# Kernel optimization log

Hardware: AMD Instinct MI355X
Metric: run time of the kernel (lower is better)

The kernel has to match this reference:

```python
import jax, jax.numpy as jnp
import numpy as np

B, H, S, D = 16, 12, 1024, 64  # batch, heads, seq, head_dim (dim=768, num_head=12)


def setup_inputs() -> dict:
    key = jax.random.key(0)
    ks = jax.random.split(key, 9)
    sc = 1.0 / np.sqrt(D)
    return {
        "x": jax.random.normal(ks[0], (B, H, S, D), dtype=jnp.float32),
        "Wq": jax.random.normal(ks[1], (D, D), dtype=jnp.float32) * sc,
        "bq": jax.random.normal(ks[2], (D,), dtype=jnp.float32) * 0.02,
        "Wk": jax.random.normal(ks[3], (D, D), dtype=jnp.float32) * sc,
        "bk": jax.random.normal(ks[4], (D,), dtype=jnp.float32) * 0.02,
        "Wv": jax.random.normal(ks[5], (D, D), dtype=jnp.float32) * sc,
        "bv": jax.random.normal(ks[6], (D,), dtype=jnp.float32) * 0.02,
        "Wo": jax.random.normal(ks[7], (D, D), dtype=jnp.float32) * sc,
        "bo": jax.random.normal(ks[8], (D,), dtype=jnp.float32) * 0.02,
    }


def reference(x, Wq, bq, Wk, bk, Wv, bv, Wo, bo):
    # torch Linear: y = x @ W^T + b, applied to last dim (head_dim)
    q = jnp.einsum("bhsd,ed->bhse", x, Wq) + bq
    k = jnp.einsum("bhsd,ed->bhse", x, Wk) + bk
    v = jnp.einsum("bhsd,ed->bhse", x, Wv) + bv
    scores = jnp.einsum("bhqd,bhkd->bhqk", q, k) / jnp.sqrt(jnp.float32(q.shape[-1]))
    attn = jax.nn.softmax(scores, axis=-1)
    out = jnp.einsum("bhqk,bhkd->bhqd", attn, v)
    out = jnp.einsum("bhsd,ed->bhse", out, Wo) + bo
    return out
```

## Files before the change

### kernel.cpp

```cpp
#include <hip/hip_runtime.h>
#include <math.h>


typedef __bf16 bf16x8 __attribute__((ext_vector_type(8)));
typedef float  f32x4  __attribute__((ext_vector_type(4)));

#define MFMA(a, b, c) __builtin_amdgcn_mfma_f32_16x16x32_bf16((a), (b), (c), 0, 0, 0)

static constexpr int S = 1024;
static constexpr int PAD = 72;
static constexpr size_t NE = 196608ull * 64ull;
static constexpr float QSCALE = 0.125f * 1.4426950408889634f;

__device__ inline unsigned long long pack4bf(float a, float b, float c, float d) {
    union { __bf16 h[4]; unsigned long long u; } pk;
    pk.h[0] = (__bf16)a; pk.h[1] = (__bf16)b; pk.h[2] = (__bf16)c; pk.h[3] = (__bf16)d;
    return pk.u;
}

union frag_u { bf16x8 v; unsigned long long u[2]; };

__global__ __launch_bounds__(256, 3) void proj(
    const float* __restrict__ x,
    const float* __restrict__ Wq, const float* __restrict__ bq,
    const float* __restrict__ Wk, const float* __restrict__ bk,
    const float* __restrict__ Wv, const float* __restrict__ bv,
    __bf16* __restrict__ gq, __bf16* __restrict__ gk, __bf16* __restrict__ gvt)
{
    __shared__ __align__(16) __bf16 lx[128][PAD];
    __shared__ __align__(16) __bf16 lbuf[128][PAD];
    __shared__ __align__(16) __bf16 lw[3][8][64][8];
    __shared__ float lb[3][64];

    const int tid = threadIdx.x;
    const int row_base = blockIdx.x * 128;

    #pragma unroll
    for (int i = tid * 4; i < 8192; i += 1024) {
        float4 v = *(const float4*)(x + (size_t)row_base * 64 + i);
        int r = i >> 6, c = i & 63;
        *(unsigned long long*)&lx[r][c] = pack4bf(v.x, v.y, v.z, v.w);
    }
    #pragma unroll
    for (int c = tid; c < 1536; c += 256) {
        int mtx = c >> 9, rest = c & 511;
        int fe = rest >> 6, ln = rest & 63;
        int mm = ln & 15, qq = ln >> 4;
        int et = fe >> 1, half = fe & 1;
        const float* src = (mtx == 0 ? Wq : mtx == 1 ? Wk : Wv)
                           + (size_t)(et * 16 + mm) * 64 + half * 32 + qq * 8;
        float4 u0 = *(const float4*)(src);
        float4 u1 = *(const float4*)(src + 4);
        *(unsigned long long*)&lw[mtx][fe][ln][0] = pack4bf(u0.x, u0.y, u0.z, u0.w);
        *(unsigned long long*)&lw[mtx][fe][ln][4] = pack4bf(u1.x, u1.y, u1.z, u1.w);
    }
    if (tid < 64) { lb[0][tid] = bq[tid]; lb[1][tid] = bk[tid]; lb[2][tid] = bv[tid]; }
    __syncthreads();

    const int w = tid >> 6, lane = tid & 63, m = lane & 15, quad = lane >> 4;
    const int bh = row_base >> 10;
    const int s_base = row_base & 1023;

    bf16x8 xf[2][2];
    #pragma unroll
    for (int g = 0; g < 2; g++) {
        xf[g][0] = *(const bf16x8*)&lx[w * 32 + g * 16 + m][quad * 8];
        xf[g][1] = *(const bf16x8*)&lx[w * 32 + g * 16 + m][32 + quad * 8];
    }

    #pragma unroll
    for (int mtx = 0; mtx < 2; mtx++) {
        #pragma unroll
        for (int et = 0; et < 4; et++) {
            bf16x8 wf0 = *(const bf16x8*)&lw[mtx][et * 2 + 0][lane][0];
            bf16x8 wf1 = *(const bf16x8*)&lw[mtx][et * 2 + 1][lane][0];
            float4 bias = *(const float4*)&lb[mtx][et * 16 + quad * 4];
            #pragma unroll
            for (int g = 0; g < 2; g++) {
                f32x4 acc = {0.f, 0.f, 0.f, 0.f};
                acc = MFMA(wf0, xf[g][0], acc);
                acc = MFMA(wf1, xf[g][1], acc);
                unsigned long long u;
                if (mtx == 0)
                    u = pack4bf((acc[0] + bias.x) * QSCALE, (acc[1] + bias.y) * QSCALE,
                                (acc[2] + bias.z) * QSCALE, (acc[3] + bias.w) * QSCALE);
                else
                    u = pack4bf(acc[0] + bias.x, acc[1] + bias.y,
                                acc[2] + bias.z, acc[3] + bias.w);
                *(unsigned long long*)&lbuf[w * 32 + g * 16 + m][et * 16 + quad * 4] = u;
            }
        }
        __syncthreads();
        __bf16* dst = (mtx == 0 ? gq : gk);
        #pragma unroll
        for (int it = 0; it < 4; it++) {
            int idx = it * 256 + tid;
            int row = idx >> 3, col = (idx & 7) * 8;
            *(uint4*)(dst + ((size_t)row_base + row) * 64 + col) = *(uint4*)&lbuf[row][col];
        }
        __syncthreads();
    }

    __bf16 (*lvt)[136] = (__bf16(*)[136])&lbuf[0][0];
    #pragma unroll
    for (int et = 0; et < 4; et++) {
        bf16x8 wf0 = *(const bf16x8*)&lw[2][et * 2 + 0][lane][0];
        bf16x8 wf1 = *(const bf16x8*)&lw[2][et * 2 + 1][lane][0];
        const float bias = lb[2][et * 16 + m];
        #pragma unroll
        for (int g = 0; g < 2; g++) {
            f32x4 acc = {0.f, 0.f, 0.f, 0.f};
            acc = MFMA(xf[g][0], wf0, acc);
            acc = MFMA(xf[g][1], wf1, acc);
            const int tp = (2 * w + g) & 3;
            const int p0 = 64 * (w >> 1) + 32 * (tp >> 1) + 8 * quad + 4 * (tp & 1);
            *(unsigned long long*)&lvt[et * 16 + m][p0] =
                pack4bf(acc[0] + bias, acc[1] + bias, acc[2] + bias, acc[3] + bias);
        }
    }
    __syncthreads();
    #pragma unroll
    for (int it = 0; it < 4; it++) {
        int idx = it * 256 + tid;
        int row = idx >> 4, col = (idx & 15) * 8;
        *(uint4*)(gvt + ((size_t)bh * 64 + row) * 1024 + s_base + col) = *(uint4*)&lvt[row][col];
    }
}

__global__ __launch_bounds__(256, 3) void attn(
    const __bf16* __restrict__ gq, const __bf16* __restrict__ gk,
    const __bf16* __restrict__ gvt, const float* __restrict__ Wo,
    const float* __restrict__ bo, float* __restrict__ out)
{
    __shared__ __align__(16) __bf16 lk[64][PAD];
    __shared__ __align__(16) __bf16 lv[64][PAD];

    const int tid = threadIdx.x;
    const int w = tid >> 6, lane = tid & 63, m = lane & 15, quad = lane >> 4;
    const int bh = blockIdx.x;
    const int q0 = blockIdx.y * 256 + w * 64;

    bf16x8 qf[4][2];
    #pragma unroll
    for (int g = 0; g < 4; g++) {
        const __bf16* qrow = gq + ((size_t)bh * S + q0 + g * 16 + m) * 64;
        qf[g][0] = *(const bf16x8*)(qrow + quad * 8);
        qf[g][1] = *(const bf16x8*)(qrow + 32 + quad * 8);
    }

    f32x4 o[4][4];
    float lsum[4] = {0.f, 0.f, 0.f, 0.f};
    #pragma unroll
    for (int g = 0; g < 4; g++)
        #pragma unroll
        for (int n = 0; n < 4; n++) o[g][n] = {0.f, 0.f, 0.f, 0.f};

    const int sr = tid >> 3;
    const int sc = (tid & 7) * 8;
    const __bf16* kbase = gk + (size_t)bh * S * 64;
    const __bf16* vbase = gvt + (size_t)bh * 64 * 1024;

    for (int kb = 0; kb < 16; kb++) {
        __syncthreads();
        {
            const int nb = kb * 64;
            uint4 k0 = *(const uint4*)(kbase + (size_t)(nb + sr) * 64 + sc);
            uint4 k1 = *(const uint4*)(kbase + (size_t)(nb + sr + 32) * 64 + sc);
            uint4 v0 = *(const uint4*)(vbase + (size_t)sr * 1024 + nb + sc);
            uint4 v1 = *(const uint4*)(vbase + (size_t)(sr + 32) * 1024 + nb + sc);
            *(uint4*)&lk[sr][sc]      = k0;
            *(uint4*)&lk[sr + 32][sc] = k1;
            *(uint4*)&lv[sr][sc]      = v0;
            *(uint4*)&lv[sr + 32][sc] = v1;
        }
        __syncthreads();

        __builtin_amdgcn_s_setprio(1);
        #pragma unroll
        for (int gp = 0; gp < 2; gp++) {
            frag_u pb[2][2];
            #pragma unroll
            for (int t = 0; t < 4; t++) {
                bf16x8 ka0 = *(const bf16x8*)&lk[t * 16 + m][quad * 8];
                bf16x8 ka1 = *(const bf16x8*)&lk[t * 16 + m][32 + quad * 8];
                #pragma unroll
                for (int gl = 0; gl < 2; gl++) {
                    const int g = gp * 2 + gl;
                    f32x4 acc = {0.f, 0.f, 0.f, 0.f};
                    acc = MFMA(ka0, qf[g][0], acc);
                    acc = MFMA(ka1, qf[g][1], acc);
                    float e0 = __builtin_amdgcn_exp2f(acc[0]);
                    float e1 = __builtin_amdgcn_exp2f(acc[1]);
                    float e2 = __builtin_amdgcn_exp2f(acc[2]);
                    float e3 = __builtin_amdgcn_exp2f(acc[3]);
                    lsum[g] += (e0 + e1) + (e2 + e3);
                    pb[gl][t >> 1].u[t & 1] = pack4bf(e0, e1, e2, e3);
                }
            }
            #pragma unroll
            for (int n = 0; n < 4; n++) {
                bf16x8 va0 = *(const bf16x8*)&lv[n * 16 + m][quad * 8];
                bf16x8 va1 = *(const bf16x8*)&lv[n * 16 + m][32 + quad * 8];
                #pragma unroll
                for (int gl = 0; gl < 2; gl++) {
                    const int g = gp * 2 + gl;
                    o[g][n] = MFMA(va0, pb[gl][0].v, o[g][n]);
                    o[g][n] = MFMA(va1, pb[gl][1].v, o[g][n]);
                }
            }
        }
        __builtin_amdgcn_s_setprio(0);
    }

    #pragma unroll
    for (int g = 0; g < 4; g++) {
        lsum[g] += __shfl_xor(lsum[g], 16);
        lsum[g] += __shfl_xor(lsum[g], 32);
    }

    bf16x8 wf[4][2];
    #pragma unroll
    for (int et = 0; et < 4; et++) {
        const float* worow = Wo + (size_t)(et * 16 + m) * 64;
        float4 c0 = *(const float4*)(worow + 4 * quad);
        float4 c1 = *(const float4*)(worow + 16 + 4 * quad);
        float4 c2 = *(const float4*)(worow + 32 + 4 * quad);
        float4 c3 = *(const float4*)(worow + 48 + 4 * quad);
        frag_u f0, f1;
        f0.u[0] = pack4bf(c0.x, c0.y, c0.z, c0.w);
        f0.u[1] = pack4bf(c1.x, c1.y, c1.z, c1.w);
        f1.u[0] = pack4bf(c2.x, c2.y, c2.z, c2.w);
        f1.u[1] = pack4bf(c3.x, c3.y, c3.z, c3.w);
        wf[et][0] = f0.v;
        wf[et][1] = f1.v;
    }
    float biasr[4];
    #pragma unroll
    for (int et = 0; et < 4; et++) biasr[et] = bo[et * 16 + m];

    #pragma unroll
    for (int g = 0; g < 4; g++) {
        const float inv = 1.f / lsum[g];
        frag_u af0, af1;
        af0.u[0] = pack4bf(o[g][0][0] * inv, o[g][0][1] * inv, o[g][0][2] * inv, o[g][0][3] * inv);
        af0.u[1] = pack4bf(o[g][1][0] * inv, o[g][1][1] * inv, o[g][1][2] * inv, o[g][1][3] * inv);
        af1.u[0] = pack4bf(o[g][2][0] * inv, o[g][2][1] * inv, o[g][2][2] * inv, o[g][2][3] * inv);
        af1.u[1] = pack4bf(o[g][3][0] * inv, o[g][3][1] * inv, o[g][3][2] * inv, o[g][3][3] * inv);
        #pragma unroll
        for (int et = 0; et < 4; et++) {
            f32x4 acc = {0.f, 0.f, 0.f, 0.f};
            acc = MFMA(af0.v, wf[et][0], acc);
            acc = MFMA(af1.v, wf[et][1], acc);
            #pragma unroll
            for (int r = 0; r < 4; r++) {
                size_t row = (size_t)bh * S + q0 + g * 16 + quad * 4 + r;
                out[row * 64 + et * 16 + m] = acc[r] + biasr[et];
            }
        }
    }
}

extern "C" void kernel_launch(void* const* d_in, const int* in_sizes, int n_in,
                              void* d_out, int out_size, void* d_ws, size_t ws_size,
                              hipStream_t stream) {
    const float* x  = (const float*)d_in[0];
    const float* Wq = (const float*)d_in[1];
    const float* bq = (const float*)d_in[2];
    const float* Wk = (const float*)d_in[3];
    const float* bk = (const float*)d_in[4];
    const float* Wv = (const float*)d_in[5];
    const float* bv = (const float*)d_in[6];
    const float* Wo = (const float*)d_in[7];
    const float* bo = (const float*)d_in[8];
    float* out = (float*)d_out;

    __bf16* gq  = (__bf16*)d_ws;
    __bf16* gk  = gq + NE;
    __bf16* gvt = gk + NE;

    proj<<<1536, 256, 0, stream>>>(x, Wq, bq, Wk, bk, Wv, bv, gq, gk, gvt);
    attn<<<dim3(192, 4), 256, 0, stream>>>(gq, gk, gvt, Wo, bo, out);
}
```

Measured before the change: 231.5 us.

## Fuse Q projection into attention kernel and double threads per block

The Q projection moves out of the projection kernel and into the attention kernel. Each attention block now loads its x rows, projects them to Q in shared memory with MFMA, and keeps Q in registers, so Q is never written to or read back from global memory. The attention block grows to 512 threads, with each wave handling 32 query rows instead of 64, which halves per-wave accumulator registers and lets one K/V tile load feed twice as many waves. The trade-off is that every attention block now loads and converts Wq and x itself, and each wave has less work per K/V tile to hide latency with.

Result: faster. 207.3 us (-10.5%).

```diff
diff --git a/kernel.cpp b/kernel.cpp
--- a/kernel.cpp
+++ b/kernel.cpp
@@ -20,17 +20,16 @@
 
 union frag_u { bf16x8 v; unsigned long long u[2]; };
 
-__global__ __launch_bounds__(256, 3) void proj(
+__global__ __launch_bounds__(256, 3) void projkv(
     const float* __restrict__ x,
-    const float* __restrict__ Wq, const float* __restrict__ bq,
     const float* __restrict__ Wk, const float* __restrict__ bk,
     const float* __restrict__ Wv, const float* __restrict__ bv,
-    __bf16* __restrict__ gq, __bf16* __restrict__ gk, __bf16* __restrict__ gvt)
+    __bf16* __restrict__ gk, __bf16* __restrict__ gvt)
 {
     __shared__ __align__(16) __bf16 lx[128][PAD];
     __shared__ __align__(16) __bf16 lbuf[128][PAD];
-    __shared__ __align__(16) __bf16 lw[3][8][64][8];
-    __shared__ float lb[3][64];
+    __shared__ __align__(16) __bf16 lw[2][8][64][8];
+    __shared__ float lb[2][64];
 
     const int tid = threadIdx.x;
     const int row_base = blockIdx.x * 128;
@@ -42,19 +41,18 @@
         *(unsigned long long*)&lx[r][c] = pack4bf(v.x, v.y, v.z, v.w);
     }
     #pragma unroll
-    for (int c = tid; c < 1536; c += 256) {
+    for (int c = tid; c < 1024; c += 256) {
         int mtx = c >> 9, rest = c & 511;
         int fe = rest >> 6, ln = rest & 63;
         int mm = ln & 15, qq = ln >> 4;
         int et = fe >> 1, half = fe & 1;
-        const float* src = (mtx == 0 ? Wq : mtx == 1 ? Wk : Wv)
-                           + (size_t)(et * 16 + mm) * 64 + half * 32 + qq * 8;
+        const float* src = (mtx ? Wv : Wk) + (size_t)(et * 16 + mm) * 64 + half * 32 + qq * 8;
         float4 u0 = *(const float4*)(src);
         float4 u1 = *(const float4*)(src + 4);
         *(unsigned long long*)&lw[mtx][fe][ln][0] = pack4bf(u0.x, u0.y, u0.z, u0.w);
         *(unsigned long long*)&lw[mtx][fe][ln][4] = pack4bf(u1.x, u1.y, u1.z, u1.w);
     }
-    if (tid < 64) { lb[0][tid] = bq[tid]; lb[1][tid] = bk[tid]; lb[2][tid] = bv[tid]; }
+    if (tid < 64) { lb[0][tid] = bk[tid]; lb[1][tid] = bv[tid]; }
     __syncthreads();
 
     const int w = tid >> 6, lane = tid & 63, m = lane & 15, quad = lane >> 4;
@@ -69,44 +67,35 @@
     }
 
     #pragma unroll
-    for (int mtx = 0; mtx < 2; mtx++) {
-        #pragma unroll
-        for (int et = 0; et < 4; et++) {
-            bf16x8 wf0 = *(const bf16x8*)&lw[mtx][et * 2 + 0][lane][0];
-            bf16x8 wf1 = *(const bf16x8*)&lw[mtx][et * 2 + 1][lane][0];
-            float4 bias = *(const float4*)&lb[mtx][et * 16 + quad * 4];
-            #pragma unroll
-            for (int g = 0; g < 2; g++) {
-                f32x4 acc = {0.f, 0.f, 0.f, 0.f};
-                acc = MFMA(wf0, xf[g][0], acc);
-                acc = MFMA(wf1, xf[g][1], acc);
-                unsigned long long u;
-                if (mtx == 0)
-                    u = pack4bf((acc[0] + bias.x) * QSCALE, (acc[1] + bias.y) * QSCALE,
-                                (acc[2] + bias.z) * QSCALE, (acc[3] + bias.w) * QSCALE);
-                else
-                    u = pack4bf(acc[0] + bias.x, acc[1] + bias.y,
-                                acc[2] + bias.z, acc[3] + bias.w);
-                *(unsigned long long*)&lbuf[w * 32 + g * 16 + m][et * 16 + quad * 4] = u;
-            }
-        }
-        __syncthreads();
-        __bf16* dst = (mtx == 0 ? gq : gk);
-        #pragma unroll
-        for (int it = 0; it < 4; it++) {
-            int idx = it * 256 + tid;
-            int row = idx >> 3, col = (idx & 7) * 8;
-            *(uint4*)(dst + ((size_t)row_base + row) * 64 + col) = *(uint4*)&lbuf[row][col];
-        }
-        __syncthreads();
-    }
+    for (int et = 0; et < 4; et++) {
+        bf16x8 wf0 = *(const bf16x8*)&lw[0][et * 2 + 0][lane][0];
+        bf16x8 wf1 = *(const bf16x8*)&lw[0][et * 2 + 1][lane][0];
+        float4 bias = *(const float4*)&lb[0][et * 16 + quad * 4];
+        #pragma unroll
+        for (int g = 0; g < 2; g++) {
+            f32x4 acc = {0.f, 0.f, 0.f, 0.f};
+            acc = MFMA(wf0, xf[g][0], acc);
+            acc = MFMA(wf1, xf[g][1], acc);
+            *(unsigned long long*)&lbuf[w * 32 + g * 16 + m][et * 16 + quad * 4] =
+                pack4bf(acc[0] + bias.x, acc[1] + bias.y,
+                        acc[2] + bias.z, acc[3] + bias.w);
+        }
+    }
+    __syncthreads();
+    #pragma unroll
+    for (int it = 0; it < 4; it++) {
+        int idx = it * 256 + tid;
+        int row = idx >> 3, col = (idx & 7) * 8;
+        *(uint4*)(gk + ((size_t)row_base + row) * 64 + col) = *(uint4*)&lbuf[row][col];
+    }
+    __syncthreads();
 
     __bf16 (*lvt)[136] = (__bf16(*)[136])&lbuf[0][0];
     #pragma unroll
     for (int et = 0; et < 4; et++) {
-        bf16x8 wf0 = *(const bf16x8*)&lw[2][et * 2 + 0][lane][0];
-        bf16x8 wf1 = *(const bf16x8*)&lw[2][et * 2 + 1][lane][0];
-        const float bias = lb[2][et * 16 + m];
+        bf16x8 wf0 = *(const bf16x8*)&lw[1][et * 2 + 0][lane][0];
+        bf16x8 wf1 = *(const bf16x8*)&lw[1][et * 2 + 1][lane][0];
+        const float bias = lb[1][et * 16 + m];
         #pragma unroll
         for (int g = 0; g < 2; g++) {
             f32x4 acc = {0.f, 0.f, 0.f, 0.f};
@@ -127,31 +116,76 @@
     }
 }
 
-__global__ __launch_bounds__(256, 3) void attn(
-    const __bf16* __restrict__ gq, const __bf16* __restrict__ gk,
-    const __bf16* __restrict__ gvt, const float* __restrict__ Wo,
-    const float* __restrict__ bo, float* __restrict__ out)
+__global__ __launch_bounds__(512, 4) void attn(
+    const float* __restrict__ x,
+    const float* __restrict__ Wq, const float* __restrict__ bq,
+    const __bf16* __restrict__ gk, const __bf16* __restrict__ gvt,
+    const float* __restrict__ Wo, const float* __restrict__ bo,
+    float* __restrict__ out)
 {
-    __shared__ __align__(16) __bf16 lk[64][PAD];
-    __shared__ __align__(16) __bf16 lv[64][PAD];
+    __shared__ __align__(16) union {
+        __bf16 xq[256][PAD];
+        struct {
+            __bf16 k[64][PAD];
+            __bf16 v[64][PAD];
+        } m;
+    } L;
 
     const int tid = threadIdx.x;
     const int w = tid >> 6, lane = tid & 63, m = lane & 15, quad = lane >> 4;
     const int bh = blockIdx.x;
-    const int q0 = blockIdx.y * 256 + w * 64;
-
-    bf16x8 qf[4][2];
-    #pragma unroll
-    for (int g = 0; g < 4; g++) {
-        const __bf16* qrow = gq + ((size_t)bh * S + q0 + g * 16 + m) * 64;
-        qf[g][0] = *(const bf16x8*)(qrow + quad * 8);
-        qf[g][1] = *(const bf16x8*)(qrow + 32 + quad * 8);
-    }
-
-    f32x4 o[4][4];
-    float lsum[4] = {0.f, 0.f, 0.f, 0.f};
-    #pragma unroll
-    for (int g = 0; g < 4; g++)
+    const int q0 = blockIdx.y * 256 + w * 32;
+
+    const float* xq32 = x + ((size_t)bh * 1024 + blockIdx.y * 256) * 64;
+    #pragma unroll
+    for (int i = tid * 4; i < 16384; i += 2048) {
+        float4 v = *(const float4*)(xq32 + i);
+        int r = i >> 6, c = i & 63;
+        *(unsigned long long*)&L.xq[r][c] = pack4bf(v.x, v.y, v.z, v.w);
+    }
+    __syncthreads();
+
+    bf16x8 xqf[2][2];
+    #pragma unroll
+    for (int g = 0; g < 2; g++) {
+        xqf[g][0] = *(const bf16x8*)&L.xq[w * 32 + g * 16 + m][quad * 8];
+        xqf[g][1] = *(const bf16x8*)&L.xq[w * 32 + g * 16 + m][32 + quad * 8];
+    }
+    #pragma unroll
+    for (int et = 0; et < 4; et++) {
+        const float* wqrow = Wq + (size_t)(et * 16 + m) * 64;
+        float4 a0 = *(const float4*)(wqrow + quad * 8);
+        float4 a1 = *(const float4*)(wqrow + quad * 8 + 4);
+        float4 a2 = *(const float4*)(wqrow + 32 + quad * 8);
+        float4 a3 = *(const float4*)(wqrow + 36 + quad * 8);
+        frag_u wf0, wf1;
+        wf0.u[0] = pack4bf(a0.x, a0.y, a0.z, a0.w);
+        wf0.u[1] = pack4bf(a1.x, a1.y, a1.z, a1.w);
+        wf1.u[0] = pack4bf(a2.x, a2.y, a2.z, a2.w);
+        wf1.u[1] = pack4bf(a3.x, a3.y, a3.z, a3.w);
+        float4 bias = *(const float4*)(bq + et * 16 + quad * 4);
+        #pragma unroll
+        for (int g = 0; g < 2; g++) {
+            f32x4 acc = {0.f, 0.f, 0.f, 0.f};
+            acc = MFMA(wf0.v, xqf[g][0], acc);
+            acc = MFMA(wf1.v, xqf[g][1], acc);
+            *(unsigned long long*)&L.xq[w * 32 + g * 16 + m][et * 16 + quad * 4] =
+                pack4bf((acc[0] + bias.x) * QSCALE, (acc[1] + bias.y) * QSCALE,
+                        (acc[2] + bias.z) * QSCALE, (acc[3] + bias.w) * QSCALE);
+        }
+    }
+    bf16x8 qf[2][2];
+    #pragma unroll
+    for (int g = 0; g < 2; g++) {
+        qf[g][0] = *(const bf16x8*)&L.xq[w * 32 + g * 16 + m][quad * 8];
+        qf[g][1] = *(const bf16x8*)&L.xq[w * 32 + g * 16 + m][32 + quad * 8];
+    }
+    __syncthreads();
+
+    f32x4 o[2][4];
+    float lsum[2] = {0.f, 0.f};
+    #pragma unroll
+    for (int g = 0; g < 2; g++)
         #pragma unroll
         for (int n = 0; n < 4; n++) o[g][n] = {0.f, 0.f, 0.f, 0.f};
 
@@ -165,55 +199,46 @@
         {
             const int nb = kb * 64;
             uint4 k0 = *(const uint4*)(kbase + (size_t)(nb + sr) * 64 + sc);
-            uint4 k1 = *(const uint4*)(kbase + (size_t)(nb + sr + 32) * 64 + sc);
             uint4 v0 = *(const uint4*)(vbase + (size_t)sr * 1024 + nb + sc);
-            uint4 v1 = *(const uint4*)(vbase + (size_t)(sr + 32) * 1024 + nb + sc);
-            *(uint4*)&lk[sr][sc]      = k0;
-            *(uint4*)&lk[sr + 32][sc] = k1;
-            *(uint4*)&lv[sr][sc]      = v0;
-            *(uint4*)&lv[sr + 32][sc] = v1;
+            *(uint4*)&L.m.k[sr][sc] = k0;
+            *(uint4*)&L.m.v[sr][sc] = v0;
         }
         __syncthreads();
 
         __builtin_amdgcn_s_setprio(1);
-        #pragma unroll
-        for (int gp = 0; gp < 2; gp++) {
-            frag_u pb[2][2];
+        frag_u pb[2][2];
+        #pragma unroll
+        for (int t = 0; t < 4; t++) {
+            bf16x8 ka0 = *(const bf16x8*)&L.m.k[t * 16 + m][quad * 8];
+            bf16x8 ka1 = *(const bf16x8*)&L.m.k[t * 16 + m][32 + quad * 8];
             #pragma unroll
-            for (int t = 0; t < 4; t++) {
-                bf16x8 ka0 = *(const bf16x8*)&lk[t * 16 + m][quad * 8];
-                bf16x8 ka1 = *(const bf16x8*)&lk[t * 16 + m][32 + quad * 8];
-                #pragma unroll
-                for (int gl = 0; gl < 2; gl++) {
-                    const int g = gp * 2 + gl;
-                    f32x4 acc = {0.f, 0.f, 0.f, 0.f};
-                    acc = MFMA(ka0, qf[g][0], acc);
-                    acc = MFMA(ka1, qf[g][1], acc);
-                    float e0 = __builtin_amdgcn_exp2f(acc[0]);
-                    float e1 = __builtin_amdgcn_exp2f(acc[1]);
-                    float e2 = __builtin_amdgcn_exp2f(acc[2]);
-                    float e3 = __builtin_amdgcn_exp2f(acc[3]);
-                    lsum[g] += (e0 + e1) + (e2 + e3);
-                    pb[gl][t >> 1].u[t & 1] = pack4bf(e0, e1, e2, e3);
-                }
+            for (int g = 0; g < 2; g++) {
+                f32x4 acc = {0.f, 0.f, 0.f, 0.f};
+                acc = MFMA(ka0, qf[g][0], acc);
+                acc = MFMA(ka1, qf[g][1], acc);
+                float e0 = __builtin_amdgcn_exp2f(acc[0]);
+                float e1 = __builtin_amdgcn_exp2f(acc[1]);
+                float e2 = __builtin_amdgcn_exp2f(acc[2]);
+                float e3 = __builtin_amdgcn_exp2f(acc[3]);
+                lsum[g] += (e0 + e1) + (e2 + e3);
+                pb[g][t >> 1].u[t & 1] = pack4bf(e0, e1, e2, e3);
             }
+        }
+        #pragma unroll
+        for (int n = 0; n < 4; n++) {
+            bf16x8 va0 = *(const bf16x8*)&L.m.v[n * 16 + m][quad * 8];
+            bf16x8 va1 = *(const bf16x8*)&L.m.v[n * 16 + m][32 + quad * 8];
             #pragma unroll
-            for (int n = 0; n < 4; n++) {
-                bf16x8 va0 = *(const bf16x8*)&lv[n * 16 + m][quad * 8];
-                bf16x8 va1 = *(const bf16x8*)&lv[n * 16 + m][32 + quad * 8];
-                #pragma unroll
-                for (int gl = 0; gl < 2; gl++) {
-                    const int g = gp * 2 + gl;
-                    o[g][n] = MFMA(va0, pb[gl][0].v, o[g][n]);
-                    o[g][n] = MFMA(va1, pb[gl][1].v, o[g][n]);
-                }
+            for (int g = 0; g < 2; g++) {
+                o[g][n] = MFMA(va0, pb[g][0].v, o[g][n]);
+                o[g][n] = MFMA(va1, pb[g][1].v, o[g][n]);
             }
         }
         __builtin_amdgcn_s_setprio(0);
     }
 
     #pragma unroll
-    for (int g = 0; g < 4; g++) {
+    for (int g = 0; g < 2; g++) {
         lsum[g] += __shfl_xor(lsum[g], 16);
         lsum[g] += __shfl_xor(lsum[g], 32);
     }
@@ -239,7 +264,7 @@
     for (int et = 0; et < 4; et++) biasr[et] = bo[et * 16 + m];
 
     #pragma unroll
-    for (int g = 0; g < 4; g++) {
+    for (int g = 0; g < 2; g++) {
         const float inv = 1.f / lsum[g];
         frag_u af0, af1;
         af0.u[0] = pack4bf(o[g][0][0] * inv, o[g][0][1] * inv, o[g][0][2] * inv, o[g][0][3] * inv);
@@ -274,10 +299,9 @@
     const float* bo = (const float*)d_in[8];
     float* out = (float*)d_out;
 
-    __bf16* gq  = (__bf16*)d_ws;
-    __bf16* gk  = gq + NE;
+    __bf16* gk  = (__bf16*)d_ws;
     __bf16* gvt = gk + NE;
 
-    proj<<<1536, 256, 0, stream>>>(x, Wq, bq, Wk, bk, Wv, bv, gq, gk, gvt);
-    attn<<<dim3(192, 4), 256, 0, stream>>>(gq, gk, gvt, Wo, bo, out);
+    projkv<<<1536, 256, 0, stream>>>(x, Wk, bk, Wv, bv, gk, gvt);
+    attn<<<dim3(192, 4), 512, 0, stream>>>(x, Wq, bq, gk, gvt, Wo, bo, out);
 }
```
